# Kernel tuning notes

Hardware: AMD Instinct MI355X
Metric: run time of the kernel (lower is better)

## Reference

```python
import jax, jax.numpy as jnp
import numpy as np

DIM = 192
NUM_TOKENS = 64
RD = 10
B, N = 32, 4096
EPS = 1e-12  # F.normalize eps


def setup_inputs() -> dict:
    key = jax.random.key(0)
    ks = jax.random.split(key, 9)
    s = 1.0 / np.sqrt(DIM)
    return {
        "x": jax.random.normal(ks[0], (B, N, DIM), dtype=jnp.float32),
        "td": jax.random.normal(ks[1], (B, NUM_TOKENS, DIM), dtype=jnp.float32),
        "wq_w": jax.random.uniform(ks[2], (RD, DIM), jnp.float32, -s, s),
        "wq_b": jax.random.uniform(ks[3], (RD,), jnp.float32, -s, s),
        "wk_w": jax.random.uniform(ks[4], (RD, DIM), jnp.float32, -s, s),
        "wk_b": jax.random.uniform(ks[5], (RD,), jnp.float32, -s, s),
        "wv_w": jax.random.uniform(ks[6], (DIM, DIM), jnp.float32, -s, s),
        "wv_b": jax.random.uniform(ks[7], (DIM,), jnp.float32, -s, s),
        "scale": jnp.ones((1,), dtype=jnp.float32),
        "x_size": 64,
    }


def _l2norm(t):
    # matches F.normalize(dim=-1, eps=1e-12): x / max(||x||, eps)
    n = jnp.sqrt(jnp.sum(t * t, axis=-1, keepdims=True))
    return t / jnp.maximum(n, EPS)


def reference(x, td, wq_w, wq_b, wk_w, wk_b, wv_w, wv_b, scale, x_size):
    # q: (b, n, dr); k: (b, m, dr); v: (b, m, c)
    q = jnp.einsum("bnc,dc->bnd", x, wq_w) + wq_b
    k = jnp.einsum("bmc,dc->bmd", td, wk_w) + wk_b
    v = jnp.einsum("bmc,ec->bme", td, wv_w) + wv_b
    # cosine similarity attention logits: (b, n, m)
    attn = jnp.einsum("bnd,bmd->bnm", _l2norm(q), _l2norm(k))
    attn = attn * (1.0 + jnp.clip(scale, 0.0, 3.0) * np.log(NUM_TOKENS))
    attn = jax.nn.softmax(attn, axis=-1)
    out = jnp.einsum("bnm,bme->bne", attn, v)  # (b, n, c)
    return out, attn
```

## Files before the change

kernel.cpp:

```cpp
#include <hip/hip_runtime.h>
#include <math.h>

#define DIM 192
#define NT 64
#define RD 10
#define BB 32
#define NN 4096
#define LN64 4.1588830833596715f

typedef __attribute__((ext_vector_type(8))) short short8v;
typedef __attribute__((ext_vector_type(4))) float float4v;

#define WQF_OFF 0
#define KNF_OFF 4096
#define VF_OFF  (4096 + 32 * 2048)

__device__ __forceinline__ ushort f2bf(float f) {
    union { float f; unsigned u; } v; v.f = f;
    unsigned r = (v.u + 0x7fffu + ((v.u >> 16) & 1u)) >> 16;
    return (ushort)r;
}

__global__ __launch_bounds__(256, 2) void ATD_prep(
        const float* __restrict__ td,
        const float* __restrict__ wk_w, const float* __restrict__ wk_b,
        const float* __restrict__ wv_w, const float* __restrict__ wv_b,
        const float* __restrict__ wq_w,
        ushort* __restrict__ wsu) {
    __shared__ float smem[15696];
    const int b = blockIdx.x, y = blockIdx.y, t = threadIdx.x;
    const float* tdb = td + (size_t)b * NT * DIM;

    if (y < 12) {
        float4* td_s = (float4*)smem;
        float4* wv_s = (float4*)(smem + 64 * 196);
        float*  wvb_s = smem + 64 * 196 + 16 * 196;

        const float4* tds = (const float4*)tdb;
        #pragma unroll
        for (int j = 0; j < 12; ++j) {
            int idx = t + 256 * j;
            td_s[(idx / 48) * 49 + (idx % 48)] = tds[idx];
        }
        const float4* wvs = (const float4*)(wv_w + (size_t)(y * 16) * DIM);
        #pragma unroll
        for (int j = 0; j < 3; ++j) {
            int idx = t + 256 * j;
            wv_s[(idx / 48) * 49 + (idx % 48)] = wvs[idx];
        }
        if (t < 16) wvb_s[t] = wv_b[y * 16 + t];
        __syncthreads();

        const int ks = t >> 7;
        const int l  = (t >> 1) & 63;
        const int ih = t & 1;
        const int mb = ks * 32 + (l >> 4) * 8 + ih * 4;
        const int e  = l & 15;

        float a0 = wvb_s[e], a1 = a0, a2 = a0, a3 = a0;
        const float4* w4 = wv_s + e * 49;
        const float4* t0 = td_s + (mb + 0) * 49;
        const float4* t1 = td_s + (mb + 1) * 49;
        const float4* t2 = td_s + (mb + 2) * 49;
        const float4* t3 = td_s + (mb + 3) * 49;
        #pragma unroll 4
        for (int c4 = 0; c4 < 48; ++c4) {
            float4 w = w4[c4];
            float4 r0 = t0[c4], r1 = t1[c4], r2 = t2[c4], r3 = t3[c4];
            a0 += r0.x * w.x + r0.y * w.y + r0.z * w.z + r0.w * w.w;
            a1 += r1.x * w.x + r1.y * w.y + r1.z * w.z + r1.w * w.w;
            a2 += r2.x * w.x + r2.y * w.y + r2.z * w.z + r2.w * w.w;
            a3 += r3.x * w.x + r3.y * w.y + r3.z * w.z + r3.w * w.w;
        }
        ushort o[4] = {f2bf(a0), f2bf(a1), f2bf(a2), f2bf(a3)};
        *(uint2*)(wsu + VF_OFF + (size_t)b * 12288 + ks * 6144 + y * 512 + l * 8 + ih * 4)
            = *(uint2*)o;
    } else {
        float* kp   = smem;
        float* kn_s = smem + 3072;

        const int m = t & 63, ch = t >> 6;
        float k[RD];
        #pragma unroll
        for (int d = 0; d < RD; ++d) k[d] = 0.f;
        const float4* td4 = (const float4*)(tdb + (size_t)m * DIM) + ch * 12;
        #pragma unroll 4
        for (int c4 = 0; c4 < 12; ++c4) {
            float4 a = td4[c4];
            #pragma unroll
            for (int d = 0; d < RD; ++d) {
                float4 w = ((const float4*)(wk_w + (size_t)d * DIM))[ch * 12 + c4];
                k[d] += a.x * w.x + a.y * w.y + a.z * w.z + a.w * w.w;
            }
        }
        #pragma unroll
        for (int d = 0; d < RD; ++d) kp[(ch * 64 + m) * 12 + d] = k[d];
        __syncthreads();
        if (t < NT) {
            float kk[RD], ss = 0.f;
            #pragma unroll
            for (int d = 0; d < RD; ++d) {
                kk[d] = wk_b[d] + kp[t * 12 + d] + kp[(64 + t) * 12 + d]
                      + kp[(128 + t) * 12 + d] + kp[(192 + t) * 12 + d];
                ss += kk[d] * kk[d];
            }
            float rn = 1.f / fmaxf(sqrtf(ss), 1e-12f);
            #pragma unroll
            for (int d = 0; d < 16; ++d)
                kn_s[t * 16 + d] = (d < RD) ? kk[d] * rn : 0.f;
        }
        __syncthreads();
        {
            int mt = t >> 6, l = t & 63;
            ushort tmp[8];
            #pragma unroll
            for (int i = 0; i < 8; ++i) {
                int d = (l >> 4) * 8 + i;
                int mm = mt * 16 + (l & 15);
                tmp[i] = (d < 16) ? f2bf(kn_s[mm * 16 + d]) : (ushort)0;
            }
            *(uint4*)(wsu + KNF_OFF + (size_t)b * 2048 + t * 8) = *(uint4*)tmp;
        }
        if (b == 0) {
            for (int s = t; s < 384; s += 256) {
                int ksq = s >> 6, l = s & 63;
                ushort tmp[8];
                #pragma unroll
                for (int i = 0; i < 8; ++i) {
                    int d = l & 15;
                    int c = ksq * 32 + (l >> 4) * 8 + i;
                    tmp[i] = (d < RD) ? f2bf(wq_w[(size_t)d * DIM + c]) : (ushort)0;
                }
                *(uint4*)(wsu + WQF_OFF + s * 8) = *(uint4*)tmp;
            }
        }
    }
}

__global__ __launch_bounds__(256, 4) void ATD_main(
        const float* __restrict__ x, const float* __restrict__ wq_b,
        const float* __restrict__ scale, const ushort* __restrict__ wsu,
        float* __restrict__ out, float* __restrict__ attn) {
    __shared__ ushort qn_lds[4][512];
    __shared__ ushort p_lds[4][1024];

    const int t = threadIdx.x, w = t >> 6, l = t & 63;
    const int b = blockIdx.y;
    const int rbase = blockIdx.x * 64 + w * 16;
    const int lg = l >> 4;
    const int lc = l & 15;

    float4 xf[12];
    {
        const float* xr = x + ((size_t)b * NN + rbase + lc) * DIM + lg * 8;
        #pragma unroll
        for (int ks = 0; ks < 6; ++ks) {
            xf[2 * ks]     = *(const float4*)(xr + ks * 32);
            xf[2 * ks + 1] = *(const float4*)(xr + ks * 32 + 4);
        }
    }

    short8v wqf[6];
    #pragma unroll
    for (int ks = 0; ks < 6; ++ks)
        wqf[ks] = *(const short8v*)(wsu + WQF_OFF + ks * 512 + l * 8);
    short8v knf[4];
    #pragma unroll
    for (int mt = 0; mt < 4; ++mt)
        knf[mt] = *(const short8v*)(wsu + KNF_OFF + (size_t)b * 2048 + mt * 512 + l * 8);

    {
        unsigned* z = (unsigned*)(&qn_lds[w][0]);
        #pragma unroll
        for (int i = 0; i < 4; ++i) z[l + 64 * i] = 0u;
    }

    const float bias = (lc < RD) ? wq_b[lc] : 0.f;
    const float factor = 1.0f + fminf(fmaxf(scale[0], 0.f), 3.f) * LN64;

    char* qnbase = (char*)(&qn_lds[w][0]);
    char* pbase  = (char*)(&p_lds[w][0]);
    const float4v z4 = {0.f, 0.f, 0.f, 0.f};

    float4v qacc = {bias, bias, bias, bias};
    #pragma unroll
    for (int ks = 0; ks < 6; ++ks) {
        float xv[8] = {xf[2 * ks].x, xf[2 * ks].y, xf[2 * ks].z, xf[2 * ks].w,
                       xf[2 * ks + 1].x, xf[2 * ks + 1].y, xf[2 * ks + 1].z, xf[2 * ks + 1].w};
        unsigned hi[4], lo[4];
        #pragma unroll
        for (int i = 0; i < 4; ++i) {
            unsigned a = __float_as_uint(xv[2 * i]);
            unsigned c = __float_as_uint(xv[2 * i + 1]);
            hi[i] = (a >> 16) | (c & 0xFFFF0000u);
            float h0 = __uint_as_float(a & 0xFFFF0000u);
            float h1 = __uint_as_float(c & 0xFFFF0000u);
            float d0 = xv[2 * i] - h0;
            float d1 = xv[2 * i + 1] - h1;
            lo[i] = (__float_as_uint(d0) >> 16) | (__float_as_uint(d1) & 0xFFFF0000u);
        }
        short8v xhi = *(short8v*)hi;
        short8v xlo = *(short8v*)lo;
        qacc = __builtin_amdgcn_mfma_f32_16x16x32_bf16(xhi, wqf[ks], qacc, 0, 0, 0);
        qacc = __builtin_amdgcn_mfma_f32_16x16x32_bf16(xlo, wqf[ks], qacc, 0, 0, 0);
    }

    float sj[4];
    #pragma unroll
    for (int j = 0; j < 4; ++j) sj[j] = qacc[j] * qacc[j];
    #pragma unroll
    for (int mm = 1; mm < 16; mm <<= 1) {
        #pragma unroll
        for (int j = 0; j < 4; ++j) sj[j] += __shfl_xor(sj[j], mm, 64);
    }
    #pragma unroll
    for (int j = 0; j < 4; ++j) {
        float rn = 1.f / fmaxf(sqrtf(sj[j]), 1e-12f);
        int row = lg * 4 + j;
        int addr = (row * 64 + lc * 2) ^ (((row >> 2) & 3) << 5);
        *(ushort*)(qnbase + addr) = f2bf(qacc[j] * rn);
    }

    float4v sA[4];
    {
        int aaddr = (lc * 64 + lg * 16) ^ (((lc >> 2) & 3) << 5);
        short8v qnA = *(short8v*)(qnbase + aaddr);
        #pragma unroll
        for (int mt = 0; mt < 4; ++mt)
            sA[mt] = __builtin_amdgcn_mfma_f32_16x16x32_bf16(qnA, knf[mt], z4, 0, 0, 0);
    }

    float mx[4], sum[4], pv[4][4];
    #pragma unroll
    for (int j = 0; j < 4; ++j)
        mx[j] = fmaxf(fmaxf(sA[0][j], sA[1][j]), fmaxf(sA[2][j], sA[3][j]));
    #pragma unroll
    for (int mm = 1; mm < 16; mm <<= 1) {
        #pragma unroll
        for (int j = 0; j < 4; ++j) mx[j] = fmaxf(mx[j], __shfl_xor(mx[j], mm, 64));
    }
    #pragma unroll
    for (int j = 0; j < 4; ++j) sum[j] = 0.f;
    #pragma unroll
    for (int mt = 0; mt < 4; ++mt) {
        #pragma unroll
        for (int j = 0; j < 4; ++j) {
            float e = __expf((sA[mt][j] - mx[j]) * factor);
            pv[mt][j] = e; sum[j] += e;
        }
    }
    #pragma unroll
    for (int mm = 1; mm < 16; mm <<= 1) {
        #pragma unroll
        for (int j = 0; j < 4; ++j) sum[j] += __shfl_xor(sum[j], mm, 64);
    }
    #pragma unroll
    for (int j = 0; j < 4; ++j) sum[j] = 1.f / sum[j];
    #pragma unroll
    for (int mt = 0; mt < 4; ++mt)
        #pragma unroll
        for (int j = 0; j < 4; ++j) pv[mt][j] *= sum[j];

    #pragma unroll
    for (int mt = 0; mt < 4; ++mt)
        #pragma unroll
        for (int j = 0; j < 4; ++j) {
            int row = lg * 4 + j;
            int m = lc + 16 * mt;
            int addr = (row * 128 + m * 2) ^ (((row >> 2) & 3) << 5);
            *(ushort*)(pbase + addr) = f2bf(pv[mt][j]);
        }

    {
        const ushort* vfb = wsu + VF_OFF + (size_t)b * 12288;
        int xorm = ((lc >> 2) & 3) << 5;
        short8v A0 = *(short8v*)(pbase + ((lc * 128 + lg * 16) ^ xorm));
        short8v A1 = *(short8v*)(pbase + ((lc * 128 + 64 + lg * 16) ^ xorm));
        float* ob = out + ((size_t)b * NN + rbase) * DIM + lc;

        short8v B0 = *(const short8v*)(vfb + l * 8);
        short8v B1 = *(const short8v*)(vfb + 6144 + l * 8);
        #pragma unroll
        for (int ct = 0; ct < 12; ++ct) {
            short8v nB0 = B0, nB1 = B1;
            if (ct < 11) {
                nB0 = *(const short8v*)(vfb + (ct + 1) * 512 + l * 8);
                nB1 = *(const short8v*)(vfb + 6144 + (ct + 1) * 512 + l * 8);
            }
            float4v acc = __builtin_amdgcn_mfma_f32_16x16x32_bf16(A0, B0, z4, 0, 0, 0);
            acc = __builtin_amdgcn_mfma_f32_16x16x32_bf16(A1, B1, acc, 0, 0, 0);
            #pragma unroll
            for (int j = 0; j < 4; ++j)
                __builtin_nontemporal_store(acc[j], &ob[(lg * 4 + j) * DIM + ct * 16]);
            B0 = nB0; B1 = nB1;
        }
    }

    {
        float* ab = attn + ((size_t)b * NN + rbase) * NT;
        #pragma unroll
        for (int mt = 0; mt < 4; ++mt)
            #pragma unroll
            for (int j = 0; j < 4; ++j)
                __builtin_nontemporal_store(pv[mt][j],
                    &ab[(lg * 4 + j) * NT + lc + 16 * mt]);
    }
}

extern "C" void kernel_launch(void* const* d_in, const int* in_sizes, int n_in,
                              void* d_out, int out_size, void* d_ws, size_t ws_size,
                              hipStream_t stream) {
    const float* x     = (const float*)d_in[0];
    const float* td    = (const float*)d_in[1];
    const float* wq_w  = (const float*)d_in[2];
    const float* wq_b  = (const float*)d_in[3];
    const float* wk_w  = (const float*)d_in[4];
    const float* wk_b  = (const float*)d_in[5];
    const float* wv_w  = (const float*)d_in[6];
    const float* wv_b  = (const float*)d_in[7];
    const float* scale = (const float*)d_in[8];

    float* out  = (float*)d_out;
    float* attn = out + (size_t)BB * NN * DIM;
    ushort* wsu = (ushort*)d_ws;

    ATD_prep<<<dim3(BB, 13), 256, 0, stream>>>(td, wk_w, wk_b, wv_w, wv_b, wq_w, wsu);
    ATD_main<<<dim3(NN / 64, BB), 256, 0, stream>>>(x, wq_b, scale, wsu, out, attn);
}
```

Before: 63.81 us.

## Process two row tiles per block and prefetch second tile's x during first

Each block now handles 128 rows as two 64-row tiles, halving the grid. The second tile's x values are loaded into registers while the first tile's softmax and PV work runs, overlapping global loads with compute, and the K and V setup is amortized across both tiles. The Wq fragments are now reloaded per k-step inside the projection instead of being held in registers. Holding two x tiles raises register pressure and could reduce occupancy, and the smaller grid gives less parallelism.

```diff
diff --git a/kernel.cpp b/kernel.cpp
--- a/kernel.cpp
+++ b/kernel.cpp
@@ -137,54 +137,21 @@
     }
 }
 
-__global__ __launch_bounds__(256, 4) void ATD_main(
-        const float* __restrict__ x, const float* __restrict__ wq_b,
-        const float* __restrict__ scale, const ushort* __restrict__ wsu,
-        float* __restrict__ out, float* __restrict__ attn) {
-    __shared__ ushort qn_lds[4][512];
-    __shared__ ushort p_lds[4][1024];
-
-    const int t = threadIdx.x, w = t >> 6, l = t & 63;
-    const int b = blockIdx.y;
-    const int rbase = blockIdx.x * 64 + w * 16;
-    const int lg = l >> 4;
-    const int lc = l & 15;
-
-    float4 xf[12];
-    {
-        const float* xr = x + ((size_t)b * NN + rbase + lc) * DIM + lg * 8;
-        #pragma unroll
-        for (int ks = 0; ks < 6; ++ks) {
-            xf[2 * ks]     = *(const float4*)(xr + ks * 32);
-            xf[2 * ks + 1] = *(const float4*)(xr + ks * 32 + 4);
-        }
-    }
-
-    short8v wqf[6];
-    #pragma unroll
-    for (int ks = 0; ks < 6; ++ks)
-        wqf[ks] = *(const short8v*)(wsu + WQF_OFF + ks * 512 + l * 8);
-    short8v knf[4];
-    #pragma unroll
-    for (int mt = 0; mt < 4; ++mt)
-        knf[mt] = *(const short8v*)(wsu + KNF_OFF + (size_t)b * 2048 + mt * 512 + l * 8);
-
-    {
-        unsigned* z = (unsigned*)(&qn_lds[w][0]);
-        #pragma unroll
-        for (int i = 0; i < 4; ++i) z[l + 64 * i] = 0u;
-    }
-
-    const float bias = (lc < RD) ? wq_b[lc] : 0.f;
-    const float factor = 1.0f + fminf(fmaxf(scale[0], 0.f), 3.f) * LN64;
-
-    char* qnbase = (char*)(&qn_lds[w][0]);
-    char* pbase  = (char*)(&p_lds[w][0]);
-    const float4v z4 = {0.f, 0.f, 0.f, 0.f};
-
+__device__ __forceinline__ void load_x(float4 (&xf)[12], const float* xr) {
+    #pragma unroll
+    for (int ks = 0; ks < 6; ++ks) {
+        xf[2 * ks]     = *(const float4*)(xr + ks * 32);
+        xf[2 * ks + 1] = *(const float4*)(xr + ks * 32 + 4);
+    }
+}
+
+__device__ __forceinline__ float4v do_qproj(const float4 (&xf)[12],
+                                            const ushort* __restrict__ wsu,
+                                            int l, float bias) {
     float4v qacc = {bias, bias, bias, bias};
     #pragma unroll
     for (int ks = 0; ks < 6; ++ks) {
+        short8v wqf = *(const short8v*)(wsu + WQF_OFF + ks * 512 + l * 8);
         float xv[8] = {xf[2 * ks].x, xf[2 * ks].y, xf[2 * ks].z, xf[2 * ks].w,
                        xf[2 * ks + 1].x, xf[2 * ks + 1].y, xf[2 * ks + 1].z, xf[2 * ks + 1].w};
         unsigned hi[4], lo[4];
@@ -201,9 +168,18 @@
         }
         short8v xhi = *(short8v*)hi;
         short8v xlo = *(short8v*)lo;
-        qacc = __builtin_amdgcn_mfma_f32_16x16x32_bf16(xhi, wqf[ks], qacc, 0, 0, 0);
-        qacc = __builtin_amdgcn_mfma_f32_16x16x32_bf16(xlo, wqf[ks], qacc, 0, 0, 0);
-    }
+        qacc = __builtin_amdgcn_mfma_f32_16x16x32_bf16(xhi, wqf, qacc, 0, 0, 0);
+        qacc = __builtin_amdgcn_mfma_f32_16x16x32_bf16(xlo, wqf, qacc, 0, 0, 0);
+    }
+    return qacc;
+}
+
+__device__ __forceinline__ void tile_tail(float4v qacc, int b, int rbase,
+        int l, int lg, int lc, char* qnbase, char* pbase,
+        const short8v (&knf)[4], float factor,
+        const ushort* __restrict__ vfb,
+        float* __restrict__ out, float* __restrict__ attn) {
+    const float4v z4 = {0.f, 0.f, 0.f, 0.f};
 
     float sj[4];
     #pragma unroll
@@ -272,7 +248,6 @@
         }
 
     {
-        const ushort* vfb = wsu + VF_OFF + (size_t)b * 12288;
         int xorm = ((lc >> 2) & 3) << 5;
         short8v A0 = *(short8v*)(pbase + ((lc * 128 + lg * 16) ^ xorm));
         short8v A1 = *(short8v*)(pbase + ((lc * 128 + 64 + lg * 16) ^ xorm));
@@ -305,6 +280,52 @@
                 __builtin_nontemporal_store(pv[mt][j],
                     &ab[(lg * 4 + j) * NT + lc + 16 * mt]);
     }
+}
+
+__global__ __launch_bounds__(256, 4) void ATD_main(
+        const float* __restrict__ x, const float* __restrict__ wq_b,
+        const float* __restrict__ scale, const ushort* __restrict__ wsu,
+        float* __restrict__ out, float* __restrict__ attn) {
+    __shared__ ushort qn_lds[4][512];
+    __shared__ ushort p_lds[4][1024];
+
+    const int t = threadIdx.x, w = t >> 6, l = t & 63;
+    const int b = blockIdx.y;
+    const int rbase0 = blockIdx.x * 128 + w * 16;
+    const int rbase1 = rbase0 + 64;
+    const int lg = l >> 4;
+    const int lc = l & 15;
+
+    float4 xfA[12];
+    load_x(xfA, x + ((size_t)b * NN + rbase0 + lc) * DIM + lg * 8);
+
+    short8v knf[4];
+    #pragma unroll
+    for (int mt = 0; mt < 4; ++mt)
+        knf[mt] = *(const short8v*)(wsu + KNF_OFF + (size_t)b * 2048 + mt * 512 + l * 8);
+
+    {
+        unsigned* z = (unsigned*)(&qn_lds[w][0]);
+        #pragma unroll
+        for (int i = 0; i < 4; ++i) z[l + 64 * i] = 0u;
+    }
+
+    const float bias = (lc < RD) ? wq_b[lc] : 0.f;
+    const float factor = 1.0f + fminf(fmaxf(scale[0], 0.f), 3.f) * LN64;
+
+    char* qnbase = (char*)(&qn_lds[w][0]);
+    char* pbase  = (char*)(&p_lds[w][0]);
+    const ushort* vfb = wsu + VF_OFF + (size_t)b * 12288;
+
+    float4v q0 = do_qproj(xfA, wsu, l, bias);
+
+    float4 xfB[12];
+    load_x(xfB, x + ((size_t)b * NN + rbase1 + lc) * DIM + lg * 8);
+
+    tile_tail(q0, b, rbase0, l, lg, lc, qnbase, pbase, knf, factor, vfb, out, attn);
+
+    float4v q1 = do_qproj(xfB, wsu, l, bias);
+    tile_tail(q1, b, rbase1, l, lg, lc, qnbase, pbase, knf, factor, vfb, out, attn);
 }
 
 extern "C" void kernel_launch(void* const* d_in, const int* in_sizes, int n_in,
@@ -325,5 +346,5 @@
     ushort* wsu = (ushort*)d_ws;
 
     ATD_prep<<<dim3(BB, 13), 256, 0, stream>>>(td, wk_w, wk_b, wv_w, wv_b, wq_w, wsu);
-    ATD_main<<<dim3(NN / 64, BB), 256, 0, stream>>>(x, wq_b, scale, wsu, out, attn);
-}
+    ATD_main<<<dim3(NN / 128, BB), 256, 0, stream>>>(x, wq_b, scale, wsu, out, attn);
+}
```

Measured after the change: 86.81 us. +36.0%, slower.

## Transpose MFMA operand roles so each lane owns a row, enabling vector stores

Applied to the files above, without the earlier changes.

Swaps the A/B operands of the score and PV MFMAs so the accumulator layout puts 4 consecutive columns of one row in each lane. Softmax reductions then need only two cross-lane shuffles instead of four per value, and the P tile is written to LDS as packed 8-byte stores with a new swizzle. Outputs and attention are written as float4 stores instead of scalar nontemporal stores. The nontemporal hint is dropped, which may change cache behaviour on the large output writes.

```diff
diff --git a/kernel.cpp b/kernel.cpp
--- a/kernel.cpp
+++ b/kernel.cpp
@@ -224,86 +224,76 @@
     float4v sA[4];
     {
         int aaddr = (lc * 64 + lg * 16) ^ (((lc >> 2) & 3) << 5);
-        short8v qnA = *(short8v*)(qnbase + aaddr);
+        short8v qnB = *(short8v*)(qnbase + aaddr);
         #pragma unroll
         for (int mt = 0; mt < 4; ++mt)
-            sA[mt] = __builtin_amdgcn_mfma_f32_16x16x32_bf16(qnA, knf[mt], z4, 0, 0, 0);
-    }
-
-    float mx[4], sum[4], pv[4][4];
-    #pragma unroll
-    for (int j = 0; j < 4; ++j)
-        mx[j] = fmaxf(fmaxf(sA[0][j], sA[1][j]), fmaxf(sA[2][j], sA[3][j]));
-    #pragma unroll
-    for (int mm = 1; mm < 16; mm <<= 1) {
-        #pragma unroll
-        for (int j = 0; j < 4; ++j) mx[j] = fmaxf(mx[j], __shfl_xor(mx[j], mm, 64));
-    }
-    #pragma unroll
-    for (int j = 0; j < 4; ++j) sum[j] = 0.f;
+            sA[mt] = __builtin_amdgcn_mfma_f32_16x16x32_bf16(knf[mt], qnB, z4, 0, 0, 0);
+    }
+
+    float pv[4][4];
+    {
+        float mx = sA[0][0];
+        #pragma unroll
+        for (int mt = 0; mt < 4; ++mt)
+            #pragma unroll
+            for (int j = 0; j < 4; ++j) mx = fmaxf(mx, sA[mt][j]);
+        mx = fmaxf(mx, __shfl_xor(mx, 16, 64));
+        mx = fmaxf(mx, __shfl_xor(mx, 32, 64));
+        float sum = 0.f;
+        #pragma unroll
+        for (int mt = 0; mt < 4; ++mt)
+            #pragma unroll
+            for (int j = 0; j < 4; ++j) {
+                float e = __expf((sA[mt][j] - mx) * factor);
+                pv[mt][j] = e; sum += e;
+            }
+        sum += __shfl_xor(sum, 16, 64);
+        sum += __shfl_xor(sum, 32, 64);
+        float inv = 1.f / sum;
+        #pragma unroll
+        for (int mt = 0; mt < 4; ++mt)
+            #pragma unroll
+            for (int j = 0; j < 4; ++j) pv[mt][j] *= inv;
+    }
+
     #pragma unroll
     for (int mt = 0; mt < 4; ++mt) {
-        #pragma unroll
-        for (int j = 0; j < 4; ++j) {
-            float e = __expf((sA[mt][j] - mx[j]) * factor);
-            pv[mt][j] = e; sum[j] += e;
-        }
-    }
-    #pragma unroll
-    for (int mm = 1; mm < 16; mm <<= 1) {
-        #pragma unroll
-        for (int j = 0; j < 4; ++j) sum[j] += __shfl_xor(sum[j], mm, 64);
-    }
-    #pragma unroll
-    for (int j = 0; j < 4; ++j) sum[j] = 1.f / sum[j];
-    #pragma unroll
-    for (int mt = 0; mt < 4; ++mt)
-        #pragma unroll
-        for (int j = 0; j < 4; ++j) pv[mt][j] *= sum[j];
-
-    #pragma unroll
-    for (int mt = 0; mt < 4; ++mt)
-        #pragma unroll
-        for (int j = 0; j < 4; ++j) {
-            int row = lg * 4 + j;
-            int m = lc + 16 * mt;
-            int addr = (row * 128 + m * 2) ^ (((row >> 2) & 3) << 5);
-            *(ushort*)(pbase + addr) = f2bf(pv[mt][j]);
-        }
+        ushort pk[4] = {f2bf(pv[mt][0]), f2bf(pv[mt][1]),
+                        f2bf(pv[mt][2]), f2bf(pv[mt][3])};
+        int addr = (lc * 128 + mt * 32 + lg * 8) ^ ((lc & 7) << 4);
+        *(uint2*)(pbase + addr) = *(uint2*)pk;
+    }
+
+    {
+        float* ab = attn + ((size_t)b * NN + rbase + lc) * NT;
+        #pragma unroll
+        for (int mt = 0; mt < 4; ++mt) {
+            float4 v4 = make_float4(pv[mt][0], pv[mt][1], pv[mt][2], pv[mt][3]);
+            *(float4*)(ab + mt * 16 + lg * 4) = v4;
+        }
+    }
 
     {
         const ushort* vfb = wsu + VF_OFF + (size_t)b * 12288;
-        int xorm = ((lc >> 2) & 3) << 5;
-        short8v A0 = *(short8v*)(pbase + ((lc * 128 + lg * 16) ^ xorm));
-        short8v A1 = *(short8v*)(pbase + ((lc * 128 + 64 + lg * 16) ^ xorm));
-        float* ob = out + ((size_t)b * NN + rbase) * DIM + lc;
-
-        short8v B0 = *(const short8v*)(vfb + l * 8);
-        short8v B1 = *(const short8v*)(vfb + 6144 + l * 8);
+        short8v pB0 = *(short8v*)(pbase + ((lc * 128 + lg * 16) ^ ((lc & 7) << 4)));
+        short8v pB1 = *(short8v*)(pbase + ((lc * 128 + 64 + lg * 16) ^ ((lc & 7) << 4)));
+        float* ob = out + ((size_t)b * NN + rbase + lc) * DIM;
+
+        short8v A0 = *(const short8v*)(vfb + l * 8);
+        short8v A1 = *(const short8v*)(vfb + 6144 + l * 8);
         #pragma unroll
         for (int ct = 0; ct < 12; ++ct) {
-            short8v nB0 = B0, nB1 = B1;
+            short8v nA0 = A0, nA1 = A1;
             if (ct < 11) {
-                nB0 = *(const short8v*)(vfb + (ct + 1) * 512 + l * 8);
-                nB1 = *(const short8v*)(vfb + 6144 + (ct + 1) * 512 + l * 8);
-            }
-            float4v acc = __builtin_amdgcn_mfma_f32_16x16x32_bf16(A0, B0, z4, 0, 0, 0);
-            acc = __builtin_amdgcn_mfma_f32_16x16x32_bf16(A1, B1, acc, 0, 0, 0);
-            #pragma unroll
-            for (int j = 0; j < 4; ++j)
-                __builtin_nontemporal_store(acc[j], &ob[(lg * 4 + j) * DIM + ct * 16]);
-            B0 = nB0; B1 = nB1;
-        }
-    }
-
-    {
-        float* ab = attn + ((size_t)b * NN + rbase) * NT;
-        #pragma unroll
-        for (int mt = 0; mt < 4; ++mt)
-            #pragma unroll
-            for (int j = 0; j < 4; ++j)
-                __builtin_nontemporal_store(pv[mt][j],
-                    &ab[(lg * 4 + j) * NT + lc + 16 * mt]);
+                nA0 = *(const short8v*)(vfb + (ct + 1) * 512 + l * 8);
+                nA1 = *(const short8v*)(vfb + 6144 + (ct + 1) * 512 + l * 8);
+            }
+            float4v acc = __builtin_amdgcn_mfma_f32_16x16x32_bf16(A0, pB0, z4, 0, 0, 0);
+            acc = __builtin_amdgcn_mfma_f32_16x16x32_bf16(A1, pB1, acc, 0, 0, 0);
+            float4 o4 = make_float4(acc[0], acc[1], acc[2], acc[3]);
+            *(float4*)(ob + ct * 16 + lg * 4) = o4;
+            A0 = nA0; A1 = nA1;
+        }
     }
 }
 
```

Measured after the change: 56.71 us (median of 2 runs). 11.1% less time.
